# Kernel optimization log

Hardware: AMD Instinct MI355X
Metric: run time of the kernel (lower is better)

## Reference

```python
import jax, jax.numpy as jnp
import numpy as np

B = 262144
SLOPE = 0.2

def _xavier(key, shape):
    # shape = (out_ch, in_ch, k); fan_in = in_ch*k, fan_out = out_ch*k
    fan_in = shape[1] * shape[2]
    fan_out = shape[0] * shape[2]
    limit = np.sqrt(6.0 / (fan_in + fan_out)).astype(np.float32)
    return jax.random.uniform(key, shape, jnp.float32, -limit, limit)

def setup_inputs() -> dict:
    key = jax.random.key(0)
    ks = jax.random.split(key, 5)
    x = jax.random.normal(ks[0], (B, 2, 16), jnp.float32)
    return {
        "x": x,
        "w_enc1": _xavier(ks[1], (4, 2, 3)), "b_enc1": jnp.zeros((4,), jnp.float32),
        "w_bneck": _xavier(ks[2], (8, 4, 3)), "b_bneck": jnp.zeros((8,), jnp.float32),
        "w_dec1": _xavier(ks[3], (4, 8, 3)), "b_dec1": jnp.zeros((4,), jnp.float32),
        "w_out": _xavier(ks[4], (2, 4, 3)), "b_out": jnp.zeros((2,), jnp.float32),
    }

def _conv1d(x, w, b, stride):
    # x: [B, C_in, L], w: [C_out, C_in, K], padding=1
    y = jax.lax.conv_general_dilated(
        x, w, window_strides=(stride,), padding=[(1, 1)],
        dimension_numbers=("NCH", "OIH", "NCH"))
    return y + b[None, :, None]

def _leaky(y):
    return jnp.where(y > 0, y, SLOPE * y)

def _upsample2(y):
    # nearest-neighbor x2 along length
    return jnp.repeat(y, 2, axis=-1)

def reference(x, w_enc1, b_enc1, w_bneck, b_bneck, w_dec1, b_dec1, w_out, b_out):
    enc1 = _leaky(_conv1d(x, w_enc1, b_enc1, 2))          # [B,4,8]
    bneck = _leaky(_conv1d(enc1, w_bneck, b_bneck, 2))    # [B,8,4]
    up1 = _upsample2(bneck)                               # [B,8,8]
    dec1 = _leaky(_conv1d(up1, w_dec1, b_dec1, 1))        # [B,4,8]
    skip = dec1 + enc1                                    # [B,4,8]
    up2 = _upsample2(skip)                                # [B,4,16]
    out = jnp.tanh(_conv1d(up2, w_out, b_out, 1))         # [B,2,16]
    return out
```

## Files before the change

kernel.cpp:

```cpp
#include <hip/hip_runtime.h>

#define SLOPE 0.2f

__device__ __forceinline__ float leaky(float v) {
    return v > 0.0f ? v : SLOPE * v;
}

__device__ __forceinline__ float fast_tanh(float v) {
    float e = __expf(2.0f * v);
    return 1.0f - 2.0f * __builtin_amdgcn_rcpf(e + 1.0f);
}

__global__ __launch_bounds__(256) void minigen_kernel(
    const float* __restrict__ x,
    const float* __restrict__ w1, const float* __restrict__ b1,
    const float* __restrict__ w2, const float* __restrict__ b2,
    const float* __restrict__ w3, const float* __restrict__ b3,
    const float* __restrict__ w4, const float* __restrict__ b4,
    float* __restrict__ out, int n)
{
    int i = blockIdx.x * blockDim.x + threadIdx.x;
    if (i >= n) return;

    float xr[32];
    const float4* xin = (const float4*)(x + (size_t)i * 32);
#pragma unroll
    for (int q = 0; q < 8; ++q) {
        float4 v = xin[q];
        xr[4*q+0] = v.x; xr[4*q+1] = v.y; xr[4*q+2] = v.z; xr[4*q+3] = v.w;
    }

    float e1[4][8];
#pragma unroll
    for (int oc = 0; oc < 4; ++oc) {
#pragma unroll
        for (int ol = 0; ol < 8; ++ol) {
            float s = b1[oc];
#pragma unroll
            for (int ic = 0; ic < 2; ++ic) {
#pragma unroll
                for (int k = 0; k < 3; ++k) {
                    int j = 2*ol - 1 + k;
                    if (j >= 0 && j < 16)
                        s += xr[ic*16 + j] * w1[(oc*2 + ic)*3 + k];
                }
            }
            e1[oc][ol] = leaky(s);
        }
    }

    float bn[8][4];
#pragma unroll
    for (int oc = 0; oc < 8; ++oc) {
#pragma unroll
        for (int ol = 0; ol < 4; ++ol) {
            float s = b2[oc];
#pragma unroll
            for (int ic = 0; ic < 4; ++ic) {
#pragma unroll
                for (int k = 0; k < 3; ++k) {
                    int j = 2*ol - 1 + k;
                    if (j >= 0 && j < 8)
                        s += e1[ic][j] * w2[(oc*4 + ic)*3 + k];
                }
            }
            bn[oc][ol] = leaky(s);
        }
    }

    float sk[4][8];
#pragma unroll
    for (int oc = 0; oc < 4; ++oc) {
#pragma unroll
        for (int ol = 0; ol < 8; ++ol) {
            float s = b3[oc];
#pragma unroll
            for (int ic = 0; ic < 8; ++ic) {
#pragma unroll
                for (int k = 0; k < 3; ++k) {
                    int j = ol - 1 + k;
                    if (j >= 0 && j < 8)
                        s += bn[ic][j >> 1] * w3[(oc*8 + ic)*3 + k];
                }
            }
            sk[oc][ol] = leaky(s) + e1[oc][ol];
        }
    }

    float o[32];
#pragma unroll
    for (int oc = 0; oc < 2; ++oc) {
#pragma unroll
        for (int ol = 0; ol < 16; ++ol) {
            float s = b4[oc];
#pragma unroll
            for (int ic = 0; ic < 4; ++ic) {
#pragma unroll
                for (int k = 0; k < 3; ++k) {
                    int j = ol - 1 + k;
                    if (j >= 0 && j < 16)
                        s += sk[ic][j >> 1] * w4[(oc*4 + ic)*3 + k];
                }
            }
            o[oc*16 + ol] = fast_tanh(s);
        }
    }

    float4* op = (float4*)(out + (size_t)i * 32);
#pragma unroll
    for (int q = 0; q < 8; ++q) {
        op[q] = make_float4(o[4*q+0], o[4*q+1], o[4*q+2], o[4*q+3]);
    }
}

extern "C" void kernel_launch(void* const* d_in, const int* in_sizes, int n_in,
                              void* d_out, int out_size, void* d_ws, size_t ws_size,
                              hipStream_t stream) {
    const float* x  = (const float*)d_in[0];
    const float* w1 = (const float*)d_in[1];
    const float* b1 = (const float*)d_in[2];
    const float* w2 = (const float*)d_in[3];
    const float* b2 = (const float*)d_in[4];
    const float* w3 = (const float*)d_in[5];
    const float* b3 = (const float*)d_in[6];
    const float* w4 = (const float*)d_in[7];
    const float* b4 = (const float*)d_in[8];
    float* out = (float*)d_out;

    int n = in_sizes[0] / 32;
    const int block = 256;
    int grid = (n + block - 1) / block;
    hipLaunchKernelGGL(minigen_kernel, dim3(grid), dim3(block), 0, stream,
                       x, w1, b1, w2, b2, w3, b3, w4, b4, out, n);
}
```

Before: 120.1 us.

## Recast conv layers as fp16 MFMA matmuls with LDS-staged coalesced IO

Each conv layer, including the upsampling and zero padding, is turned into a dense 32x32 Toeplitz-style matrix built in LDS per block. The four layers then run as 16x16x32 fp16 MFMA ops over batches of samples, with activations reshuffled between layers through ds_bpermute. Input and output go through a padded LDS tile so global float4 accesses are coalesced. This removes the per-thread scalar FMA chains. In exchange it uses fp16 inputs, which lowers accuracy, and it assumes the batch size is divisible by 256 with no bounds check.

```diff
diff --git a/kernel.cpp b/kernel.cpp
--- a/kernel.cpp
+++ b/kernel.cpp
@@ -1,115 +1,170 @@
 #include <hip/hip_runtime.h>
+
+typedef __attribute__((ext_vector_type(8))) _Float16 f16x8;
+typedef __attribute__((ext_vector_type(4))) float    f32x4;
+typedef __attribute__((ext_vector_type(4))) int      i32x4;
 
 #define SLOPE 0.2f
 
-__device__ __forceinline__ float leaky(float v) {
-    return v > 0.0f ? v : SLOPE * v;
+__device__ __forceinline__ int pk2(float lo, float hi) {
+    _Float16 a = (_Float16)lo, b = (_Float16)hi;
+    unsigned short ua = __builtin_bit_cast(unsigned short, a);
+    unsigned short ub = __builtin_bit_cast(unsigned short, b);
+    return (int)((unsigned)ua | ((unsigned)ub << 16));
 }
 
+__device__ __forceinline__ f32x4 lrelu4(f32x4 v) {
+    return __builtin_elementwise_max(v, SLOPE * v);
+}
 __device__ __forceinline__ float fast_tanh(float v) {
     float e = __expf(2.0f * v);
     return 1.0f - 2.0f * __builtin_amdgcn_rcpf(e + 1.0f);
 }
 
-__global__ __launch_bounds__(256) void minigen_kernel(
+__device__ __forceinline__ f16x8 xchg(f32x4 lo, f32x4 hi, int a01, int a23,
+                                      bool hiq) {
+    int P0 = pk2(lo.x, lo.y), P1 = pk2(lo.z, lo.w);
+    int P2 = pk2(hi.x, hi.y), P3 = pk2(hi.z, hi.w);
+    int e0 = __builtin_amdgcn_ds_bpermute(a01, P0);
+    int f0 = __builtin_amdgcn_ds_bpermute(a01, P2);
+    int e1 = __builtin_amdgcn_ds_bpermute(a01, P1);
+    int f1 = __builtin_amdgcn_ds_bpermute(a01, P3);
+    int e2 = __builtin_amdgcn_ds_bpermute(a23, P0);
+    int f2 = __builtin_amdgcn_ds_bpermute(a23, P2);
+    int e3 = __builtin_amdgcn_ds_bpermute(a23, P1);
+    int f3 = __builtin_amdgcn_ds_bpermute(a23, P3);
+    i32x4 r = { hiq ? f0 : e0, hiq ? f1 : e1, hiq ? f2 : e2, hiq ? f3 : e3 };
+    return __builtin_bit_cast(f16x8, r);
+}
+
+__global__ __launch_bounds__(256, 4) void minigen_kernel(
     const float* __restrict__ x,
     const float* __restrict__ w1, const float* __restrict__ b1,
     const float* __restrict__ w2, const float* __restrict__ b2,
     const float* __restrict__ w3, const float* __restrict__ b3,
     const float* __restrict__ w4, const float* __restrict__ b4,
-    float* __restrict__ out, int n)
+    float* __restrict__ out)
 {
-    int i = blockIdx.x * blockDim.x + threadIdx.x;
-    if (i >= n) return;
+    __shared__ __align__(16) float sdata[256 * 36];
+    __shared__ __align__(16) _Float16 atab[4][32 * 32];
+    __shared__ __align__(16) float btab[4][32];
 
-    float xr[32];
-    const float4* xin = (const float4*)(x + (size_t)i * 32);
+    const int t = threadIdx.x;
+    const int lane = t & 63;
+    const int w = t >> 6;
+    const int n = lane & 15, q = lane >> 4;
+    const int blockBase = blockIdx.x * 2048;
+
+    {
+        const int L = w;
 #pragma unroll
-    for (int q = 0; q < 8; ++q) {
-        float4 v = xin[q];
-        xr[4*q+0] = v.x; xr[4*q+1] = v.y; xr[4*q+2] = v.z; xr[4*q+3] = v.w;
+        for (int i = 0; i < 16; ++i) {
+            int idx = (lane << 4) + i;
+            int m = idx >> 5, k = idx & 31;
+            float v = 0.0f;
+            if (L == 0) {
+                int oc = m >> 3, l = m & 7, ic = k >> 4, j = k & 15;
+                int t3 = j - 2 * l + 1;
+                if (t3 >= 0 && t3 < 3) v = w1[(oc * 2 + ic) * 3 + t3];
+            } else if (L == 1) {
+                int oc = m >> 2, l = m & 3, ic = k >> 3, j = k & 7;
+                int t3 = j - 2 * l + 1;
+                if (t3 >= 0 && t3 < 3) v = w2[(oc * 4 + ic) * 3 + t3];
+            } else if (L == 2) {
+                int oc = m >> 3, l = m & 7, ic = k >> 2, j = k & 3;
+                for (int t3 = 0; t3 < 3; ++t3) {
+                    int u = l - 1 + t3;
+                    if (u >= 0 && u < 8 && (u >> 1) == j)
+                        v += w3[(oc * 8 + ic) * 3 + t3];
+                }
+            } else {
+                int oc = m >> 4, l = m & 15, ic = k >> 3, j = k & 7;
+                for (int t3 = 0; t3 < 3; ++t3) {
+                    int u = l - 1 + t3;
+                    if (u >= 0 && u < 16 && (u >> 1) == j)
+                        v += w4[(oc * 4 + ic) * 3 + t3];
+                }
+            }
+            atab[L][(m << 5) + k] = (_Float16)v;
+        }
+    }
+    if (t < 128) {
+        int L = t >> 5, m = t & 31;
+        float b;
+        if (L == 0)      b = b1[m >> 3];
+        else if (L == 1) b = b2[m >> 2];
+        else if (L == 2) b = b3[m >> 3];
+        else             b = b4[m >> 4];
+        btab[L][m] = b;
     }
 
-    float e1[4][8];
+    const float4* xin = (const float4*)x;
+    float4* s4 = (float4*)sdata;
 #pragma unroll
-    for (int oc = 0; oc < 4; ++oc) {
+    for (int qq = 0; qq < 8; ++qq) {
+        int g = qq * 256 + t;
+        s4[(g >> 3) * 9 + (g & 7)] = xin[blockBase + g];
+    }
+    __syncthreads();
+
+    f16x8 A[4][2];
+    f32x4 CB[4][2];
 #pragma unroll
-        for (int ol = 0; ol < 8; ++ol) {
-            float s = b1[oc];
+    for (int L = 0; L < 4; ++L)
 #pragma unroll
-            for (int ic = 0; ic < 2; ++ic) {
+        for (int h = 0; h < 2; ++h) {
+            A[L][h]  = *(const f16x8*)&atab[L][(n + 16 * h) * 32 + q * 8];
+            CB[L][h] = *(const f32x4*)&btab[L][16 * h + q * 4];
+        }
+
+    const int q2  = (q < 2) ? q : q - 2;
+    const int a01 = (n + 32 * q2) * 4;
+    const int a23 = a01 + 64;
+    const bool hiq = (q >= 2);
+
 #pragma unroll
-                for (int k = 0; k < 3; ++k) {
-                    int j = 2*ol - 1 + k;
-                    if (j >= 0 && j < 16)
-                        s += xr[ic*16 + j] * w1[(oc*2 + ic)*3 + k];
-                }
-            }
-            e1[oc][ol] = leaky(s);
-        }
+    for (int g = 0; g < 4; ++g) {
+        float* xrow = sdata + (w * 64 + g * 16 + n) * 36;
+
+        f32x4 xa = *(const f32x4*)(xrow + 8 * q);
+        f32x4 xb = *(const f32x4*)(xrow + 8 * q + 4);
+        i32x4 bi = { pk2(xa.x, xa.y), pk2(xa.z, xa.w),
+                     pk2(xb.x, xb.y), pk2(xb.z, xb.w) };
+        f16x8 B = __builtin_bit_cast(f16x8, bi);
+
+        f32x4 d0 = __builtin_amdgcn_mfma_f32_16x16x32_f16(A[0][0], B, CB[0][0], 0, 0, 0);
+        f32x4 d1 = __builtin_amdgcn_mfma_f32_16x16x32_f16(A[0][1], B, CB[0][1], 0, 0, 0);
+        d0 = lrelu4(d0); d1 = lrelu4(d1);
+        f32x4 e1lo = d0, e1hi = d1;
+
+        B = xchg(d0, d1, a01, a23, hiq);
+        d0 = __builtin_amdgcn_mfma_f32_16x16x32_f16(A[1][0], B, CB[1][0], 0, 0, 0);
+        d1 = __builtin_amdgcn_mfma_f32_16x16x32_f16(A[1][1], B, CB[1][1], 0, 0, 0);
+        d0 = lrelu4(d0); d1 = lrelu4(d1);
+
+        B = xchg(d0, d1, a01, a23, hiq);
+        d0 = __builtin_amdgcn_mfma_f32_16x16x32_f16(A[2][0], B, CB[2][0], 0, 0, 0);
+        d1 = __builtin_amdgcn_mfma_f32_16x16x32_f16(A[2][1], B, CB[2][1], 0, 0, 0);
+        d0 = lrelu4(d0) + e1lo; d1 = lrelu4(d1) + e1hi;
+
+        B = xchg(d0, d1, a01, a23, hiq);
+        d0 = __builtin_amdgcn_mfma_f32_16x16x32_f16(A[3][0], B, CB[3][0], 0, 0, 0);
+        d1 = __builtin_amdgcn_mfma_f32_16x16x32_f16(A[3][1], B, CB[3][1], 0, 0, 0);
+        f32x4 o0 = { fast_tanh(d0.x), fast_tanh(d0.y),
+                     fast_tanh(d0.z), fast_tanh(d0.w) };
+        f32x4 o1 = { fast_tanh(d1.x), fast_tanh(d1.y),
+                     fast_tanh(d1.z), fast_tanh(d1.w) };
+
+        *(f32x4*)(xrow + 4 * q)      = o0;
+        *(f32x4*)(xrow + 16 + 4 * q) = o1;
     }
+    __syncthreads();
 
-    float bn[8][4];
+    float4* outp = (float4*)out;
 #pragma unroll
-    for (int oc = 0; oc < 8; ++oc) {
-#pragma unroll
-        for (int ol = 0; ol < 4; ++ol) {
-            float s = b2[oc];
-#pragma unroll
-            for (int ic = 0; ic < 4; ++ic) {
-#pragma unroll
-                for (int k = 0; k < 3; ++k) {
-                    int j = 2*ol - 1 + k;
-                    if (j >= 0 && j < 8)
-                        s += e1[ic][j] * w2[(oc*4 + ic)*3 + k];
-                }
-            }
-            bn[oc][ol] = leaky(s);
-        }
-    }
-
-    float sk[4][8];
-#pragma unroll
-    for (int oc = 0; oc < 4; ++oc) {
-#pragma unroll
-        for (int ol = 0; ol < 8; ++ol) {
-            float s = b3[oc];
-#pragma unroll
-            for (int ic = 0; ic < 8; ++ic) {
-#pragma unroll
-                for (int k = 0; k < 3; ++k) {
-                    int j = ol - 1 + k;
-                    if (j >= 0 && j < 8)
-                        s += bn[ic][j >> 1] * w3[(oc*8 + ic)*3 + k];
-                }
-            }
-            sk[oc][ol] = leaky(s) + e1[oc][ol];
-        }
-    }
-
-    float o[32];
-#pragma unroll
-    for (int oc = 0; oc < 2; ++oc) {
-#pragma unroll
-        for (int ol = 0; ol < 16; ++ol) {
-            float s = b4[oc];
-#pragma unroll
-            for (int ic = 0; ic < 4; ++ic) {
-#pragma unroll
-                for (int k = 0; k < 3; ++k) {
-                    int j = ol - 1 + k;
-                    if (j >= 0 && j < 16)
-                        s += sk[ic][j >> 1] * w4[(oc*4 + ic)*3 + k];
-                }
-            }
-            o[oc*16 + ol] = fast_tanh(s);
-        }
-    }
-
-    float4* op = (float4*)(out + (size_t)i * 32);
-#pragma unroll
-    for (int q = 0; q < 8; ++q) {
-        op[q] = make_float4(o[4*q+0], o[4*q+1], o[4*q+2], o[4*q+3]);
+    for (int qq = 0; qq < 8; ++qq) {
+        int g = qq * 256 + t;
+        outp[blockBase + g] = s4[(g >> 3) * 9 + (g & 7)];
     }
 }
 
@@ -128,8 +183,7 @@
     float* out = (float*)d_out;
 
     int n = in_sizes[0] / 32;
-    const int block = 256;
-    int grid = (n + block - 1) / block;
-    hipLaunchKernelGGL(minigen_kernel, dim3(grid), dim3(block), 0, stream,
-                       x, w1, b1, w2, b2, w3, b3, w4, b4, out, n);
+    int grid = n / 256;
+    hipLaunchKernelGGL(minigen_kernel, dim3(grid), dim3(256), 0, stream,
+                       x, w1, b1, w2, b2, w3, b3, w4, b4, out);
 }
```

Result: faster. 112.5 us (-6.3%).

## Split each sample across four lanes with DPP halo exchange and LDS-staged coalesced IO

Applied to the files above, without the earlier changes.

Each sample is now handled by four lanes instead of one: every lane computes a quarter of the length positions and gets neighbouring boundary values from adjacent lanes through DPP row shifts. Input and output are staged through padded LDS tiles so the global float4 loads and stores are fully coalesced, rather than each thread striding over 128 bytes. This lowers per-thread register pressure and improves memory access patterns, at the cost of two block barriers and some redundant halo work. The bounds check was removed and the grid assumes the batch divides evenly by 64.

```diff
diff --git a/kernel.cpp b/kernel.cpp
--- a/kernel.cpp
+++ b/kernel.cpp
@@ -3,113 +3,168 @@
 #define SLOPE 0.2f
 
 __device__ __forceinline__ float leaky(float v) {
-    return v > 0.0f ? v : SLOPE * v;
+    return __builtin_fmaxf(v, SLOPE * v);
 }
-
 __device__ __forceinline__ float fast_tanh(float v) {
     float e = __expf(2.0f * v);
     return 1.0f - 2.0f * __builtin_amdgcn_rcpf(e + 1.0f);
 }
 
-__global__ __launch_bounds__(256) void minigen_kernel(
+__device__ __forceinline__ float qprev(float v) {
+    int i = __builtin_bit_cast(int, v);
+    i = __builtin_amdgcn_mov_dpp(i, 0x93, 0xF, 0xF, true);
+    return __builtin_bit_cast(float, i);
+}
+__device__ __forceinline__ float qnext(float v) {
+    int i = __builtin_bit_cast(int, v);
+    i = __builtin_amdgcn_mov_dpp(i, 0x39, 0xF, 0xF, true);
+    return __builtin_bit_cast(float, i);
+}
+
+__global__ __launch_bounds__(256, 8) void minigen_kernel(
     const float* __restrict__ x,
     const float* __restrict__ w1, const float* __restrict__ b1,
     const float* __restrict__ w2, const float* __restrict__ b2,
     const float* __restrict__ w3, const float* __restrict__ b3,
     const float* __restrict__ w4, const float* __restrict__ b4,
-    float* __restrict__ out, int n)
+    float* __restrict__ out)
 {
-    int i = blockIdx.x * blockDim.x + threadIdx.x;
-    if (i >= n) return;
+    __shared__ float4 lds[64 * 9];
 
-    float xr[32];
-    const float4* xin = (const float4*)(x + (size_t)i * 32);
+    const int t = threadIdx.x;
+    const int p = t & 3;
+    const int sb = t >> 2;
+    const int base = blockIdx.x * 512;
+
+    const float4* xin = (const float4*)x;
+    lds[(t >> 3) * 9 + (t & 7)] = xin[base + t];
+    {
+        int g = 256 + t;
+        lds[(g >> 3) * 9 + (g & 7)] = xin[base + g];
+    }
+    __syncthreads();
+
+    float xr[2][4];
 #pragma unroll
-    for (int q = 0; q < 8; ++q) {
-        float4 v = xin[q];
-        xr[4*q+0] = v.x; xr[4*q+1] = v.y; xr[4*q+2] = v.z; xr[4*q+3] = v.w;
+    for (int ic = 0; ic < 2; ++ic) {
+        float4 v = lds[sb * 9 + ic * 4 + p];
+        xr[ic][0] = v.x; xr[ic][1] = v.y; xr[ic][2] = v.z; xr[ic][3] = v.w;
     }
 
-    float e1[4][8];
+    float xh[2];
+#pragma unroll
+    for (int ic = 0; ic < 2; ++ic) {
+        float h = qprev(xr[ic][3]);
+        xh[ic] = p ? h : 0.0f;
+    }
+    float e1q[4][2];
 #pragma unroll
     for (int oc = 0; oc < 4; ++oc) {
 #pragma unroll
-        for (int ol = 0; ol < 8; ++ol) {
+        for (int dl = 0; dl < 2; ++dl) {
             float s = b1[oc];
 #pragma unroll
-            for (int ic = 0; ic < 2; ++ic) {
+            for (int ic = 0; ic < 2; ++ic)
 #pragma unroll
                 for (int k = 0; k < 3; ++k) {
-                    int j = 2*ol - 1 + k;
-                    if (j >= 0 && j < 16)
-                        s += xr[ic*16 + j] * w1[(oc*2 + ic)*3 + k];
+                    int u = 2 * dl - 1 + k;
+                    float v = (u < 0) ? xh[ic] : xr[ic][u];
+                    s = fmaf(v, w1[(oc * 2 + ic) * 3 + k], s);
                 }
-            }
-            e1[oc][ol] = leaky(s);
+            e1q[oc][dl] = leaky(s);
         }
     }
 
-    float bn[8][4];
+    float eh[4];
+#pragma unroll
+    for (int ic = 0; ic < 4; ++ic) {
+        float h = qprev(e1q[ic][1]);
+        eh[ic] = p ? h : 0.0f;
+    }
+    float bn[8];
 #pragma unroll
     for (int oc = 0; oc < 8; ++oc) {
+        float s = b2[oc];
 #pragma unroll
-        for (int ol = 0; ol < 4; ++ol) {
-            float s = b2[oc];
-#pragma unroll
-            for (int ic = 0; ic < 4; ++ic) {
-#pragma unroll
-                for (int k = 0; k < 3; ++k) {
-                    int j = 2*ol - 1 + k;
-                    if (j >= 0 && j < 8)
-                        s += e1[ic][j] * w2[(oc*4 + ic)*3 + k];
-                }
-            }
-            bn[oc][ol] = leaky(s);
+        for (int ic = 0; ic < 4; ++ic) {
+            s = fmaf(eh[ic],      w2[(oc * 4 + ic) * 3 + 0], s);
+            s = fmaf(e1q[ic][0],  w2[(oc * 4 + ic) * 3 + 1], s);
+            s = fmaf(e1q[ic][1],  w2[(oc * 4 + ic) * 3 + 2], s);
         }
+        bn[oc] = leaky(s);
     }
 
-    float sk[4][8];
+    float bl[8], br[8];
+#pragma unroll
+    for (int ic = 0; ic < 8; ++ic) {
+        float hl = qprev(bn[ic]);
+        float hr = qnext(bn[ic]);
+        bl[ic] = p ? hl : 0.0f;
+        br[ic] = (p == 3) ? 0.0f : hr;
+    }
+    float skq[4][2];
 #pragma unroll
     for (int oc = 0; oc < 4; ++oc) {
+        float s0 = b3[oc];
+        float s1 = b3[oc];
 #pragma unroll
-        for (int ol = 0; ol < 8; ++ol) {
-            float s = b3[oc];
-#pragma unroll
-            for (int ic = 0; ic < 8; ++ic) {
-#pragma unroll
-                for (int k = 0; k < 3; ++k) {
-                    int j = ol - 1 + k;
-                    if (j >= 0 && j < 8)
-                        s += bn[ic][j >> 1] * w3[(oc*8 + ic)*3 + k];
-                }
-            }
-            sk[oc][ol] = leaky(s) + e1[oc][ol];
+        for (int ic = 0; ic < 8; ++ic) {
+            const float* wr = w3 + (oc * 8 + ic) * 3;
+            s0 = fmaf(bl[ic], wr[0], s0);
+            s0 = fmaf(bn[ic], wr[1], s0);
+            s0 = fmaf(bn[ic], wr[2], s0);
+            s1 = fmaf(bn[ic], wr[0], s1);
+            s1 = fmaf(bn[ic], wr[1], s1);
+            s1 = fmaf(br[ic], wr[2], s1);
         }
+        skq[oc][0] = leaky(s0) + e1q[oc][0];
+        skq[oc][1] = leaky(s1) + e1q[oc][1];
     }
 
-    float o[32];
+    float sl[4], sr[4];
+#pragma unroll
+    for (int ic = 0; ic < 4; ++ic) {
+        float hl = qprev(skq[ic][1]);
+        float hr = qnext(skq[ic][0]);
+        sl[ic] = p ? hl : 0.0f;
+        sr[ic] = (p == 3) ? 0.0f : hr;
+    }
+    float o[2][4];
 #pragma unroll
     for (int oc = 0; oc < 2; ++oc) {
+        float a0 = b4[oc], a1 = b4[oc], a2 = b4[oc], a3 = b4[oc];
 #pragma unroll
-        for (int ol = 0; ol < 16; ++ol) {
-            float s = b4[oc];
-#pragma unroll
-            for (int ic = 0; ic < 4; ++ic) {
-#pragma unroll
-                for (int k = 0; k < 3; ++k) {
-                    int j = ol - 1 + k;
-                    if (j >= 0 && j < 16)
-                        s += sk[ic][j >> 1] * w4[(oc*4 + ic)*3 + k];
-                }
-            }
-            o[oc*16 + ol] = fast_tanh(s);
+        for (int ic = 0; ic < 4; ++ic) {
+            const float* wr = w4 + (oc * 4 + ic) * 3;
+            float s0 = skq[ic][0], s1 = skq[ic][1];
+            a0 = fmaf(sl[ic], wr[0], a0);
+            a0 = fmaf(s0,     wr[1], a0);
+            a0 = fmaf(s0,     wr[2], a0);
+            a1 = fmaf(s0,     wr[0], a1);
+            a1 = fmaf(s0,     wr[1], a1);
+            a1 = fmaf(s1,     wr[2], a1);
+            a2 = fmaf(s0,     wr[0], a2);
+            a2 = fmaf(s1,     wr[1], a2);
+            a2 = fmaf(s1,     wr[2], a2);
+            a3 = fmaf(s1,     wr[0], a3);
+            a3 = fmaf(s1,     wr[1], a3);
+            a3 = fmaf(sr[ic], wr[2], a3);
         }
+        o[oc][0] = fast_tanh(a0); o[oc][1] = fast_tanh(a1);
+        o[oc][2] = fast_tanh(a2); o[oc][3] = fast_tanh(a3);
     }
 
-    float4* op = (float4*)(out + (size_t)i * 32);
 #pragma unroll
-    for (int q = 0; q < 8; ++q) {
-        op[q] = make_float4(o[4*q+0], o[4*q+1], o[4*q+2], o[4*q+3]);
+    for (int oc = 0; oc < 2; ++oc)
+        lds[sb * 9 + oc * 4 + p] =
+            make_float4(o[oc][0], o[oc][1], o[oc][2], o[oc][3]);
+    __syncthreads();
+
+    float4* outp = (float4*)out;
+    outp[base + t] = lds[(t >> 3) * 9 + (t & 7)];
+    {
+        int g = 256 + t;
+        outp[base + g] = lds[(g >> 3) * 9 + (g & 7)];
     }
 }
 
@@ -128,8 +183,7 @@
     float* out = (float*)d_out;
 
     int n = in_sizes[0] / 32;
-    const int block = 256;
-    int grid = (n + block - 1) / block;
-    hipLaunchKernelGGL(minigen_kernel, dim3(grid), dim3(block), 0, stream,
-                       x, w1, b1, w2, b2, w3, b3, w4, b4, out, n);
+    int grid = n / 64;
+    hipLaunchKernelGGL(minigen_kernel, dim3(grid), dim3(256), 0, stream,
+                       x, w1, b1, w2, b2, w3, b3, w4, b4, out);
 }
```

Measured after the change: 106.1 us. 11.7% less time.
